# Optimization experiments

Measured on AMD Instinct MI355X. Metric: run time of the kernel, lower is better.

The kernel has to match this reference:

```python
import jax, jax.numpy as jnp
import numpy as np

N, E, D_F, D_H = 100000, 1600000, 128, 128


def setup_inputs() -> dict:
    key = jax.random.key(0)
    ks = jax.random.split(key, 16)
    inp = {
        'h': jax.random.normal(ks[0], (N, D_H), dtype=jnp.float32),
        'f_src': jax.random.normal(ks[1], (N, D_F), dtype=jnp.float32),
        'f_dst': jax.random.normal(ks[2], (N, D_F), dtype=jnp.float32),
        'src': jax.random.randint(ks[3], (E,), 0, N, dtype=jnp.int32),
        'dst': jax.random.randint(ks[4], (E,), 0, N, dtype=jnp.int32),
        # parameters (match torch init: 0.001*rand for W/U, zeros for b)
        'wz': 0.001 * jax.random.uniform(ks[5], (D_F, D_H), dtype=jnp.float32),
        'uz': 0.001 * jax.random.uniform(ks[6], (D_H, D_H), dtype=jnp.float32),
        'bz': jnp.zeros((1, D_H), dtype=jnp.float32),
        'wr': 0.001 * jax.random.uniform(ks[7], (D_F, D_H), dtype=jnp.float32),
        'ur': 0.001 * jax.random.uniform(ks[8], (D_H, D_H), dtype=jnp.float32),
        'br': jnp.zeros((1, D_H), dtype=jnp.float32),
        'w': 0.001 * jax.random.uniform(ks[9], (D_F, D_H), dtype=jnp.float32),
        'u': 0.001 * jax.random.uniform(ks[10], (D_H, D_H), dtype=jnp.float32),
        'b': jnp.zeros((1, D_H), dtype=jnp.float32),
    }
    return inp


def reference(h, f_src, f_dst, src, dst, wz, uz, bz, wr, ur, br, w, u, b):
    n = h.shape[0]
    # Stage 1: s[v] = sum_{u in N_in(v)} h[u]   (copy_src + sum reduce)
    s = jax.ops.segment_sum(h[src], dst, num_segments=n)  # [N, d_h]
    # z gate per node
    z = jax.nn.sigmoid(f_src @ wz + s @ uz + bz)
    # Stage 2: per-edge reset gate using SOURCE node data, then sum to dst
    h_e = h[src]                                           # [E, d_h]
    r = jax.nn.sigmoid(f_dst[src] @ wr + h_e @ ur + br)    # [E, d_h]
    sum_r_times_h = jax.ops.segment_sum(r * h_e, dst, num_segments=n)
    # Candidate state and gated update
    h_tilde = jnp.tanh(f_src @ w + sum_r_times_h @ u + b)
    h_new = (1.0 - z) * s + z * h_tilde
    return h_new
```

## Files before the change

kernel.cpp:

```cpp
#include <hip/hip_runtime.h>
#include <stdint.h>

#define DH 128

typedef __attribute__((ext_vector_type(8))) short short8;
typedef __attribute__((ext_vector_type(4))) float f32x4;

__device__ __forceinline__ unsigned short f2bf(float f) {
  union { float f; unsigned u; } v; v.f = f;
  unsigned r = v.u + 0x7fffu + ((v.u >> 16) & 1u);
  return (unsigned short)(r >> 16);
}
__device__ __forceinline__ float bf2f(unsigned short s) {
  union { unsigned u; float f; } v; v.u = ((unsigned)s) << 16;
  return v.f;
}

__global__ __launch_bounds__(256) void pack_weights(
    const float* __restrict__ wz, const float* __restrict__ uz,
    const float* __restrict__ wr, const float* __restrict__ ur,
    const float* __restrict__ w,  const float* __restrict__ u,
    unsigned short* __restrict__ wf) {
  int t = blockIdx.x * 256 + threadIdx.x;
  if (t >= 6 * 16384) return;
  int mat = t >> 14;
  int r = t & 16383;
  int j = r & 7;
  int lane = (r >> 3) & 63;
  int nt = (r >> 9) & 7;
  int kt = (r >> 12) & 3;
  int k = kt * 32 + ((lane >> 4) << 3) + j;
  int n = nt * 16 + (lane & 15);
  const float* m_;
  switch (mat) {
    case 0: m_ = wz; break; case 1: m_ = uz; break; case 2: m_ = wr; break;
    case 3: m_ = ur; break; case 4: m_ = w;  break; default: m_ = u;
  }
  wf[t] = f2bf(m_[k * DH + n]);
}

__global__ __launch_bounds__(256) void zero_counts(int* __restrict__ cnt, int N) {
  int i = blockIdx.x * 256 + threadIdx.x;
  if (i < N) cnt[i] = 0;
}
__global__ __launch_bounds__(256) void count_deg(const int* __restrict__ dst,
                                                 int* __restrict__ cnt, int E) {
  int i = blockIdx.x * 256 + threadIdx.x;
  if (i < E) atomicAdd(&cnt[dst[i]], 1);
}
__global__ __launch_bounds__(256) void block_reduce(const int* __restrict__ cnt,
                                                    int* __restrict__ bsum, int N) {
  __shared__ int sd[256];
  int t = threadIdx.x;
  int i = blockIdx.x * 256 + t;
  sd[t] = (i < N) ? cnt[i] : 0;
  __syncthreads();
  for (int d = 128; d > 0; d >>= 1) {
    if (t < d) sd[t] += sd[t + d];
    __syncthreads();
  }
  if (t == 0) bsum[blockIdx.x] = sd[0];
}
__global__ __launch_bounds__(512) void scan_bsums(int* __restrict__ bsum, int nb,
                                                  int* __restrict__ offs, int N, int E) {
  __shared__ int sd[512];
  int t = threadIdx.x;
  int v = (t < nb) ? bsum[t] : 0;
  sd[t] = v;
  __syncthreads();
  for (int d = 1; d < 512; d <<= 1) {
    int x = sd[t];
    if (t >= d) x += sd[t - d];
    __syncthreads();
    sd[t] = x;
    __syncthreads();
  }
  if (t < nb) bsum[t] = sd[t] - v;
  if (t == 0) offs[N] = E;
}
__global__ __launch_bounds__(256) void scan_block(const int* __restrict__ cnt,
                                                  const int* __restrict__ boff,
                                                  int* __restrict__ offs,
                                                  int* __restrict__ cursor, int N) {
  __shared__ int sd[256];
  int t = threadIdx.x;
  int i = blockIdx.x * 256 + t;
  int v = (i < N) ? cnt[i] : 0;
  sd[t] = v;
  __syncthreads();
  for (int d = 1; d < 256; d <<= 1) {
    int x = sd[t];
    if (t >= d) x += sd[t - d];
    __syncthreads();
    sd[t] = x;
    __syncthreads();
  }
  if (i < N) {
    int o = boff[blockIdx.x] + sd[t] - v;
    offs[i] = o;
    cursor[i] = o;
  }
}
__global__ __launch_bounds__(256) void scatter_edges(const int* __restrict__ src,
                                                     const int* __restrict__ dst,
                                                     int* __restrict__ cursor,
                                                     int* __restrict__ esrc, int E) {
  int i = blockIdx.x * 256 + threadIdx.x;
  if (i < E) {
    int pos = atomicAdd(&cursor[dst[i]], 1);
    esrc[pos] = src[i];
  }
}

__device__ __forceinline__ short8 load_afrag(const float* __restrict__ base, int row, int ko) {
  const float* p = base + (size_t)row * DH + ko;
  float4 a = *(const float4*)p;
  float4 b = *(const float4*)(p + 4);
  union { short8 v; unsigned short s[8]; } u;
  u.s[0] = f2bf(a.x); u.s[1] = f2bf(a.y); u.s[2] = f2bf(a.z); u.s[3] = f2bf(a.w);
  u.s[4] = f2bf(b.x); u.s[5] = f2bf(b.y); u.s[6] = f2bf(b.z); u.s[7] = f2bf(b.w);
  return u.v;
}

__global__ __launch_bounds__(256) void k1_node_gate(
    const float* __restrict__ fdst, const float* __restrict__ h,
    const unsigned short* __restrict__ wf, const float* __restrict__ br,
    unsigned short* __restrict__ m, int N) {
  const unsigned short* wrf = wf + 2 * 16384;
  const unsigned short* urf = wf + 3 * 16384;
  int lane = threadIdx.x & 63, wid = threadIdx.x >> 6;
  int rowb = blockIdx.x * 64 + wid * 16;
  int mrow = lane & 15, g = lane >> 4;
  int arow = rowb + mrow; if (arow > N - 1) arow = N - 1;
  f32x4 acc[8];
#pragma unroll
  for (int i = 0; i < 8; ++i) acc[i] = (f32x4){0.f, 0.f, 0.f, 0.f};
#pragma unroll
  for (int kh = 0; kh < 2; ++kh) {
    const float* srcm = kh ? h : fdst;
    const unsigned short* bfm = kh ? urf : wrf;
#pragma unroll
    for (int kt = 0; kt < 4; ++kt) {
      short8 af = load_afrag(srcm, arow, kt * 32 + g * 8);
#pragma unroll
      for (int nt = 0; nt < 8; ++nt) {
        short8 bf = *(const short8*)&bfm[(kt * 8 + nt) * 512 + lane * 8];
        acc[nt] = __builtin_amdgcn_mfma_f32_16x16x32_bf16(af, bf, acc[nt], 0, 0, 0);
      }
    }
  }
  int orow = rowb + g * 4;
#pragma unroll
  for (int nt = 0; nt < 8; ++nt) {
    int col = nt * 16 + mrow;
    float bias = br[col];
#pragma unroll
    for (int r = 0; r < 4; ++r) {
      int row = orow + r;
      if (row < N) {
        float arg = acc[nt][r] + bias;
        float gv = 1.f / (1.f + __expf(-arg));
        float mv = gv * h[(size_t)row * DH + col];
        m[(size_t)row * DH + col] = f2bf(mv);
      }
    }
  }
}

__global__ __launch_bounds__(256) void k3_gather(
    const int* __restrict__ offs, const int* __restrict__ esrc,
    const float* __restrict__ h, const unsigned short* __restrict__ m,
    float* __restrict__ s, float* __restrict__ mrh, int N) {
  int lane = threadIdx.x & 63, wid = threadIdx.x >> 6;
  int v = blockIdx.x * 4 + wid;
  if (v >= N) return;
  int e0 = offs[v], e1 = offs[v + 1];
  float sx = 0.f, sy = 0.f, mx = 0.f, my = 0.f;
  size_t c = (size_t)lane * 2;
  int e = e0;
  for (; e + 1 < e1; e += 2) {
    int u0 = esrc[e], u1 = esrc[e + 1];
    float2 h0 = *(const float2*)&h[(size_t)u0 * DH + c];
    float2 h1 = *(const float2*)&h[(size_t)u1 * DH + c];
    uint32_t m0 = *(const uint32_t*)&m[(size_t)u0 * DH + c];
    uint32_t m1 = *(const uint32_t*)&m[(size_t)u1 * DH + c];
    sx += h0.x + h1.x;
    sy += h0.y + h1.y;
    mx += bf2f((unsigned short)(m0 & 0xffff)) + bf2f((unsigned short)(m1 & 0xffff));
    my += bf2f((unsigned short)(m0 >> 16)) + bf2f((unsigned short)(m1 >> 16));
  }
  if (e < e1) {
    int u0 = esrc[e];
    float2 h0 = *(const float2*)&h[(size_t)u0 * DH + c];
    uint32_t m0 = *(const uint32_t*)&m[(size_t)u0 * DH + c];
    sx += h0.x; sy += h0.y;
    mx += bf2f((unsigned short)(m0 & 0xffff));
    my += bf2f((unsigned short)(m0 >> 16));
  }
  float2 so; so.x = sx; so.y = sy;
  float2 mo; mo.x = mx; mo.y = my;
  *(float2*)&s[(size_t)v * DH + c] = so;
  *(float2*)&mrh[(size_t)v * DH + c] = mo;
}

__global__ __launch_bounds__(256) void k4_update(
    const float* __restrict__ fsrc, const float* __restrict__ s,
    const float* __restrict__ mrh, const unsigned short* __restrict__ wf,
    const float* __restrict__ bz, const float* __restrict__ bb,
    float* __restrict__ out, int N) {
  const unsigned short* wzf = wf + 0 * 16384;
  const unsigned short* uzf = wf + 1 * 16384;
  const unsigned short* wwf = wf + 4 * 16384;
  const unsigned short* uuf = wf + 5 * 16384;
  int lane = threadIdx.x & 63, wid = threadIdx.x >> 6;
  int rowb = blockIdx.x * 64 + wid * 16;
  int mrow = lane & 15, g = lane >> 4;
  int arow = rowb + mrow; if (arow > N - 1) arow = N - 1;
  f32x4 az[8], ah[8];
#pragma unroll
  for (int i = 0; i < 8; ++i) {
    az[i] = (f32x4){0.f, 0.f, 0.f, 0.f};
    ah[i] = (f32x4){0.f, 0.f, 0.f, 0.f};
  }
#pragma unroll
  for (int kt = 0; kt < 4; ++kt) {
    short8 af = load_afrag(fsrc, arow, kt * 32 + g * 8);
#pragma unroll
    for (int nt = 0; nt < 8; ++nt) {
      short8 b0 = *(const short8*)&wzf[(kt * 8 + nt) * 512 + lane * 8];
      short8 b1 = *(const short8*)&wwf[(kt * 8 + nt) * 512 + lane * 8];
      az[nt] = __builtin_amdgcn_mfma_f32_16x16x32_bf16(af, b0, az[nt], 0, 0, 0);
      ah[nt] = __builtin_amdgcn_mfma_f32_16x16x32_bf16(af, b1, ah[nt], 0, 0, 0);
    }
  }
#pragma unroll
  for (int kt = 0; kt < 4; ++kt) {
    short8 af = load_afrag(s, arow, kt * 32 + g * 8);
#pragma unroll
    for (int nt = 0; nt < 8; ++nt) {
      short8 b0 = *(const short8*)&uzf[(kt * 8 + nt) * 512 + lane * 8];
      az[nt] = __builtin_amdgcn_mfma_f32_16x16x32_bf16(af, b0, az[nt], 0, 0, 0);
    }
  }
#pragma unroll
  for (int kt = 0; kt < 4; ++kt) {
    short8 af = load_afrag(mrh, arow, kt * 32 + g * 8);
#pragma unroll
    for (int nt = 0; nt < 8; ++nt) {
      short8 b1 = *(const short8*)&uuf[(kt * 8 + nt) * 512 + lane * 8];
      ah[nt] = __builtin_amdgcn_mfma_f32_16x16x32_bf16(af, b1, ah[nt], 0, 0, 0);
    }
  }
  int orow = rowb + g * 4;
#pragma unroll
  for (int nt = 0; nt < 8; ++nt) {
    int col = nt * 16 + mrow;
    float bzc = bz[col], bbc = bb[col];
#pragma unroll
    for (int r = 0; r < 4; ++r) {
      int row = orow + r;
      if (row < N) {
        float zarg = az[nt][r] + bzc;
        float z = 1.f / (1.f + __expf(-zarg));
        float e2 = __expf(2.f * (ah[nt][r] + bbc));
        float th = (e2 - 1.f) / (e2 + 1.f);
        float sv = s[(size_t)row * DH + col];
        out[(size_t)row * DH + col] = (1.f - z) * sv + z * th;
      }
    }
  }
}

extern "C" void kernel_launch(void* const* d_in, const int* in_sizes, int n_in,
                              void* d_out, int out_size, void* d_ws, size_t ws_size,
                              hipStream_t stream) {
  const float* h    = (const float*)d_in[0];
  const float* fsrc = (const float*)d_in[1];
  const float* fdst = (const float*)d_in[2];
  const int*   src  = (const int*)d_in[3];
  const int*   dst  = (const int*)d_in[4];
  const float* wz   = (const float*)d_in[5];
  const float* uz   = (const float*)d_in[6];
  const float* bz   = (const float*)d_in[7];
  const float* wr   = (const float*)d_in[8];
  const float* ur   = (const float*)d_in[9];
  const float* br   = (const float*)d_in[10];
  const float* w    = (const float*)d_in[11];
  const float* u    = (const float*)d_in[12];
  const float* b    = (const float*)d_in[13];
  int N = in_sizes[0] / DH;
  int E = in_sizes[3];
  float* out = (float*)d_out;

  char* ws = (char*)d_ws;
  size_t o = 0;
  auto take = [&](size_t bytes) {
    char* p = ws + o;
    o = (o + bytes + 255) & ~(size_t)255;
    return p;
  };
  unsigned short* wf     = (unsigned short*)take(6 * 16384 * sizeof(unsigned short));
  unsigned short* mbuf   = (unsigned short*)take((size_t)N * DH * 2);
  float*          mrh    = (float*)take((size_t)N * DH * 4);
  int*            cnt    = (int*)take((size_t)N * 4);
  int*            offs   = (int*)take((size_t)(N + 1) * 4);
  int*            cursor = (int*)take((size_t)N * 4);
  int*            bsum   = (int*)take(4096);
  int*            esrc   = (int*)take((size_t)E * 4);

  int nb = (N + 255) / 256;

  pack_weights<<<(6 * 16384 + 255) / 256, 256, 0, stream>>>(wz, uz, wr, ur, w, u, wf);
  zero_counts<<<nb, 256, 0, stream>>>(cnt, N);
  count_deg<<<(E + 255) / 256, 256, 0, stream>>>(dst, cnt, E);
  block_reduce<<<nb, 256, 0, stream>>>(cnt, bsum, N);
  scan_bsums<<<1, 512, 0, stream>>>(bsum, nb, offs, N, E);
  scan_block<<<nb, 256, 0, stream>>>(cnt, bsum, offs, cursor, N);
  scatter_edges<<<(E + 255) / 256, 256, 0, stream>>>(src, dst, cursor, esrc, E);
  k1_node_gate<<<(N + 63) / 64, 256, 0, stream>>>(fdst, h, wf, br, mbuf, N);
  k3_gather<<<(N + 3) / 4, 256, 0, stream>>>(offs, esrc, h, mbuf, out, mrh, N);
  k4_update<<<(N + 63) / 64, 256, 0, stream>>>(fsrc, out, mrh, wf, bz, b, out, N);
}
```

Measured before the change: 681.8 us.

## Store mrh as bf16, unroll gather by 4, use packed bf16 conversion

The intermediate sum of r*h is now written by the gather kernel as bf16 instead of fp32, and the update kernel loads it directly as an MFMA fragment without converting. This halves that buffer's write and read traffic. The gather loop is unrolled to four edges per iteration to keep more loads in flight, and the fp32-to-bf16 conversions now use the hardware packed convert instruction. The risk is a small precision loss on mrh, though it was already being rounded to bf16 before the matmul.

```diff
diff --git a/kernel.cpp b/kernel.cpp
--- a/kernel.cpp
+++ b/kernel.cpp
@@ -11,9 +11,16 @@
   unsigned r = v.u + 0x7fffu + ((v.u >> 16) & 1u);
   return (unsigned short)(r >> 16);
 }
-__device__ __forceinline__ float bf2f(unsigned short s) {
-  union { unsigned u; float f; } v; v.u = ((unsigned)s) << 16;
-  return v.f;
+__device__ __forceinline__ uint32_t cvtpk_bf16(float lo, float hi) {
+  uint32_t r;
+  asm("v_cvt_pk_bf16_f32 %0, %1, %2" : "=v"(r) : "v"(lo), "v"(hi));
+  return r;
+}
+__device__ __forceinline__ float bflo(uint32_t u) {
+  union { uint32_t u; float f; } v; v.u = u << 16; return v.f;
+}
+__device__ __forceinline__ float bfhi(uint32_t u) {
+  union { uint32_t u; float f; } v; v.u = u & 0xffff0000u; return v.f;
 }
 
 __global__ __launch_bounds__(256) void pack_weights(
@@ -116,10 +123,16 @@
   const float* p = base + (size_t)row * DH + ko;
   float4 a = *(const float4*)p;
   float4 b = *(const float4*)(p + 4);
-  union { short8 v; unsigned short s[8]; } u;
-  u.s[0] = f2bf(a.x); u.s[1] = f2bf(a.y); u.s[2] = f2bf(a.z); u.s[3] = f2bf(a.w);
-  u.s[4] = f2bf(b.x); u.s[5] = f2bf(b.y); u.s[6] = f2bf(b.z); u.s[7] = f2bf(b.w);
-  return u.v;
+  union { short8 v; uint32_t u[4]; } r;
+  r.u[0] = cvtpk_bf16(a.x, a.y);
+  r.u[1] = cvtpk_bf16(a.z, a.w);
+  r.u[2] = cvtpk_bf16(b.x, b.y);
+  r.u[3] = cvtpk_bf16(b.z, b.w);
+  return r.v;
+}
+__device__ __forceinline__ short8 load_afrag_bf(const unsigned short* __restrict__ base,
+                                                int row, int ko) {
+  return *(const short8*)(base + (size_t)row * DH + ko);
 }
 
 __global__ __launch_bounds__(256) void k1_node_gate(
@@ -170,42 +183,44 @@
 __global__ __launch_bounds__(256) void k3_gather(
     const int* __restrict__ offs, const int* __restrict__ esrc,
     const float* __restrict__ h, const unsigned short* __restrict__ m,
-    float* __restrict__ s, float* __restrict__ mrh, int N) {
+    float* __restrict__ s, unsigned short* __restrict__ mrh, int N) {
   int lane = threadIdx.x & 63, wid = threadIdx.x >> 6;
   int v = blockIdx.x * 4 + wid;
   if (v >= N) return;
   int e0 = offs[v], e1 = offs[v + 1];
   float sx = 0.f, sy = 0.f, mx = 0.f, my = 0.f;
-  size_t c = (size_t)lane * 2;
+  size_t c = (size_t)(lane * 2);
   int e = e0;
-  for (; e + 1 < e1; e += 2) {
-    int u0 = esrc[e], u1 = esrc[e + 1];
+  for (; e + 3 < e1; e += 4) {
+    int u0 = esrc[e], u1 = esrc[e + 1], u2 = esrc[e + 2], u3 = esrc[e + 3];
     float2 h0 = *(const float2*)&h[(size_t)u0 * DH + c];
     float2 h1 = *(const float2*)&h[(size_t)u1 * DH + c];
+    float2 h2 = *(const float2*)&h[(size_t)u2 * DH + c];
+    float2 h3 = *(const float2*)&h[(size_t)u3 * DH + c];
     uint32_t m0 = *(const uint32_t*)&m[(size_t)u0 * DH + c];
     uint32_t m1 = *(const uint32_t*)&m[(size_t)u1 * DH + c];
-    sx += h0.x + h1.x;
-    sy += h0.y + h1.y;
-    mx += bf2f((unsigned short)(m0 & 0xffff)) + bf2f((unsigned short)(m1 & 0xffff));
-    my += bf2f((unsigned short)(m0 >> 16)) + bf2f((unsigned short)(m1 >> 16));
-  }
-  if (e < e1) {
+    uint32_t m2 = *(const uint32_t*)&m[(size_t)u2 * DH + c];
+    uint32_t m3 = *(const uint32_t*)&m[(size_t)u3 * DH + c];
+    sx += (h0.x + h1.x) + (h2.x + h3.x);
+    sy += (h0.y + h1.y) + (h2.y + h3.y);
+    mx += (bflo(m0) + bflo(m1)) + (bflo(m2) + bflo(m3));
+    my += (bfhi(m0) + bfhi(m1)) + (bfhi(m2) + bfhi(m3));
+  }
+  for (; e < e1; ++e) {
     int u0 = esrc[e];
     float2 h0 = *(const float2*)&h[(size_t)u0 * DH + c];
     uint32_t m0 = *(const uint32_t*)&m[(size_t)u0 * DH + c];
     sx += h0.x; sy += h0.y;
-    mx += bf2f((unsigned short)(m0 & 0xffff));
-    my += bf2f((unsigned short)(m0 >> 16));
+    mx += bflo(m0); my += bfhi(m0);
   }
   float2 so; so.x = sx; so.y = sy;
-  float2 mo; mo.x = mx; mo.y = my;
   *(float2*)&s[(size_t)v * DH + c] = so;
-  *(float2*)&mrh[(size_t)v * DH + c] = mo;
+  *(uint32_t*)&mrh[(size_t)v * DH + c] = cvtpk_bf16(mx, my);
 }
 
 __global__ __launch_bounds__(256) void k4_update(
     const float* __restrict__ fsrc, const float* __restrict__ s,
-    const float* __restrict__ mrh, const unsigned short* __restrict__ wf,
+    const unsigned short* __restrict__ mrh, const unsigned short* __restrict__ wf,
     const float* __restrict__ bz, const float* __restrict__ bb,
     float* __restrict__ out, int N) {
   const unsigned short* wzf = wf + 0 * 16384;
@@ -244,7 +259,7 @@
   }
 #pragma unroll
   for (int kt = 0; kt < 4; ++kt) {
-    short8 af = load_afrag(mrh, arow, kt * 32 + g * 8);
+    short8 af = load_afrag_bf(mrh, arow, kt * 32 + g * 8);
 #pragma unroll
     for (int nt = 0; nt < 8; ++nt) {
       short8 b1 = *(const short8*)&uuf[(kt * 8 + nt) * 512 + lane * 8];
@@ -301,7 +316,7 @@
   };
   unsigned short* wf     = (unsigned short*)take(6 * 16384 * sizeof(unsigned short));
   unsigned short* mbuf   = (unsigned short*)take((size_t)N * DH * 2);
-  float*          mrh    = (float*)take((size_t)N * DH * 4);
+  unsigned short* mrh    = (unsigned short*)take((size_t)N * DH * 2);
   int*            cnt    = (int*)take((size_t)N * 4);
   int*            offs   = (int*)take((size_t)(N + 1) * 4);
   int*            cursor = (int*)take((size_t)N * 4);
```

Measured after the change: 673.7 us. No clear change (-1.2%).

## Switch to fp16 MFMA and gather interleaved fp16 h/m rows

Applied to the files above, without the earlier changes.

Weights and A-fragments now use fp16 with the f16 MFMA, converted through packed round-toward-zero instructions. The node-gate kernel writes an interleaved fp16 buffer holding h and r*h for each node, so the gather reads one 8-byte chunk per edge instead of separate fp32 h and bf16 m reads. That halves random gather traffic and stores the mrh intermediate in fp16. The gather is unrolled by four with vectorized index loads, and the degree count is vectorized with a memset instead of a zero kernel. The cost is precision: h summed from fp16 values, and fp16 accumulation of the m sum in the gather, which risks error or overflow on high-degree nodes.

```diff
diff --git a/kernel.cpp b/kernel.cpp
--- a/kernel.cpp
+++ b/kernel.cpp
@@ -3,24 +3,16 @@
 
 #define DH 128
 
-typedef __attribute__((ext_vector_type(8))) short short8;
+typedef __attribute__((ext_vector_type(8))) _Float16 half8;
+typedef __attribute__((ext_vector_type(2))) _Float16 half2v;
+typedef __attribute__((ext_vector_type(2))) __fp16 fp16x2;
 typedef __attribute__((ext_vector_type(4))) float f32x4;
-
-__device__ __forceinline__ unsigned short f2bf(float f) {
-  union { float f; unsigned u; } v; v.f = f;
-  unsigned r = v.u + 0x7fffu + ((v.u >> 16) & 1u);
-  return (unsigned short)(r >> 16);
-}
-__device__ __forceinline__ float bf2f(unsigned short s) {
-  union { unsigned u; float f; } v; v.u = ((unsigned)s) << 16;
-  return v.f;
-}
 
 __global__ __launch_bounds__(256) void pack_weights(
     const float* __restrict__ wz, const float* __restrict__ uz,
     const float* __restrict__ wr, const float* __restrict__ ur,
     const float* __restrict__ w,  const float* __restrict__ u,
-    unsigned short* __restrict__ wf) {
+    _Float16* __restrict__ wf) {
   int t = blockIdx.x * 256 + threadIdx.x;
   if (t >= 6 * 16384) return;
   int mat = t >> 14;
@@ -36,17 +28,21 @@
     case 0: m_ = wz; break; case 1: m_ = uz; break; case 2: m_ = wr; break;
     case 3: m_ = ur; break; case 4: m_ = w;  break; default: m_ = u;
   }
-  wf[t] = f2bf(m_[k * DH + n]);
-}
-
-__global__ __launch_bounds__(256) void zero_counts(int* __restrict__ cnt, int N) {
-  int i = blockIdx.x * 256 + threadIdx.x;
-  if (i < N) cnt[i] = 0;
-}
+  wf[t] = (_Float16)m_[k * DH + n];
+}
+
 __global__ __launch_bounds__(256) void count_deg(const int* __restrict__ dst,
                                                  int* __restrict__ cnt, int E) {
-  int i = blockIdx.x * 256 + threadIdx.x;
-  if (i < E) atomicAdd(&cnt[dst[i]], 1);
+  int i = (blockIdx.x * 256 + threadIdx.x) * 4;
+  if (i + 3 < E) {
+    int4 d = *(const int4*)&dst[i];
+    atomicAdd(&cnt[d.x], 1);
+    atomicAdd(&cnt[d.y], 1);
+    atomicAdd(&cnt[d.z], 1);
+    atomicAdd(&cnt[d.w], 1);
+  } else {
+    for (; i < E; ++i) atomicAdd(&cnt[dst[i]], 1);
+  }
 }
 __global__ __launch_bounds__(256) void block_reduce(const int* __restrict__ cnt,
                                                     int* __restrict__ bsum, int N) {
@@ -112,22 +108,28 @@
   }
 }
 
-__device__ __forceinline__ short8 load_afrag(const float* __restrict__ base, int row, int ko) {
+__device__ __forceinline__ half8 load_afrag(const float* __restrict__ base, int row, int ko) {
   const float* p = base + (size_t)row * DH + ko;
   float4 a = *(const float4*)p;
   float4 b = *(const float4*)(p + 4);
-  union { short8 v; unsigned short s[8]; } u;
-  u.s[0] = f2bf(a.x); u.s[1] = f2bf(a.y); u.s[2] = f2bf(a.z); u.s[3] = f2bf(a.w);
-  u.s[4] = f2bf(b.x); u.s[5] = f2bf(b.y); u.s[6] = f2bf(b.z); u.s[7] = f2bf(b.w);
-  return u.v;
+  union { half8 v; fp16x2 h[4]; } r;
+  r.h[0] = __builtin_amdgcn_cvt_pkrtz(a.x, a.y);
+  r.h[1] = __builtin_amdgcn_cvt_pkrtz(a.z, a.w);
+  r.h[2] = __builtin_amdgcn_cvt_pkrtz(b.x, b.y);
+  r.h[3] = __builtin_amdgcn_cvt_pkrtz(b.z, b.w);
+  return r.v;
+}
+__device__ __forceinline__ half8 load_afrag_h(const _Float16* __restrict__ base,
+                                              int row, int ko) {
+  return *(const half8*)(base + (size_t)row * DH + ko);
 }
 
 __global__ __launch_bounds__(256) void k1_node_gate(
     const float* __restrict__ fdst, const float* __restrict__ h,
-    const unsigned short* __restrict__ wf, const float* __restrict__ br,
-    unsigned short* __restrict__ m, int N) {
-  const unsigned short* wrf = wf + 2 * 16384;
-  const unsigned short* urf = wf + 3 * 16384;
+    const _Float16* __restrict__ wf, const float* __restrict__ br,
+    _Float16* __restrict__ hm, int N) {
+  const _Float16* wrf = wf + 2 * 16384;
+  const _Float16* urf = wf + 3 * 16384;
   int lane = threadIdx.x & 63, wid = threadIdx.x >> 6;
   int rowb = blockIdx.x * 64 + wid * 16;
   int mrow = lane & 15, g = lane >> 4;
@@ -138,14 +140,14 @@
 #pragma unroll
   for (int kh = 0; kh < 2; ++kh) {
     const float* srcm = kh ? h : fdst;
-    const unsigned short* bfm = kh ? urf : wrf;
+    const _Float16* bfm = kh ? urf : wrf;
 #pragma unroll
     for (int kt = 0; kt < 4; ++kt) {
-      short8 af = load_afrag(srcm, arow, kt * 32 + g * 8);
+      half8 af = load_afrag(srcm, arow, kt * 32 + g * 8);
 #pragma unroll
       for (int nt = 0; nt < 8; ++nt) {
-        short8 bf = *(const short8*)&bfm[(kt * 8 + nt) * 512 + lane * 8];
-        acc[nt] = __builtin_amdgcn_mfma_f32_16x16x32_bf16(af, bf, acc[nt], 0, 0, 0);
+        half8 bf = *(const half8*)&bfm[(kt * 8 + nt) * 512 + lane * 8];
+        acc[nt] = __builtin_amdgcn_mfma_f32_16x16x32_f16(af, bf, acc[nt], 0, 0, 0);
       }
     }
   }
@@ -158,10 +160,13 @@
     for (int r = 0; r < 4; ++r) {
       int row = orow + r;
       if (row < N) {
+        float hval = h[(size_t)row * DH + col];
         float arg = acc[nt][r] + bias;
         float gv = 1.f / (1.f + __expf(-arg));
-        float mv = gv * h[(size_t)row * DH + col];
-        m[(size_t)row * DH + col] = f2bf(mv);
+        float mv = gv * hval;
+        size_t base = (size_t)row * 256 + (size_t)((col >> 1) << 2) + (col & 1);
+        hm[base] = (_Float16)hval;
+        hm[base + 2] = (_Float16)mv;
       }
     }
   }
@@ -169,49 +174,52 @@
 
 __global__ __launch_bounds__(256) void k3_gather(
     const int* __restrict__ offs, const int* __restrict__ esrc,
-    const float* __restrict__ h, const unsigned short* __restrict__ m,
-    float* __restrict__ s, float* __restrict__ mrh, int N) {
+    const _Float16* __restrict__ hm,
+    float* __restrict__ s, _Float16* __restrict__ mrh, int N) {
   int lane = threadIdx.x & 63, wid = threadIdx.x >> 6;
   int v = blockIdx.x * 4 + wid;
   if (v >= N) return;
   int e0 = offs[v], e1 = offs[v + 1];
-  float sx = 0.f, sy = 0.f, mx = 0.f, my = 0.f;
-  size_t c = (size_t)lane * 2;
+  float sx = 0.f, sy = 0.f;
+  half2v msum = (half2v)(_Float16)0.f;
+  int c4 = lane * 4;
   int e = e0;
-  for (; e + 1 < e1; e += 2) {
-    int u0 = esrc[e], u1 = esrc[e + 1];
-    float2 h0 = *(const float2*)&h[(size_t)u0 * DH + c];
-    float2 h1 = *(const float2*)&h[(size_t)u1 * DH + c];
-    uint32_t m0 = *(const uint32_t*)&m[(size_t)u0 * DH + c];
-    uint32_t m1 = *(const uint32_t*)&m[(size_t)u1 * DH + c];
-    sx += h0.x + h1.x;
-    sy += h0.y + h1.y;
-    mx += bf2f((unsigned short)(m0 & 0xffff)) + bf2f((unsigned short)(m1 & 0xffff));
-    my += bf2f((unsigned short)(m0 >> 16)) + bf2f((unsigned short)(m1 >> 16));
-  }
-  if (e < e1) {
+  for (; e + 3 < e1; e += 4) {
+    int4 uu = *(const int4*)&esrc[e];
+    uint2 q0 = *(const uint2*)(hm + (size_t)uu.x * 256 + c4);
+    uint2 q1 = *(const uint2*)(hm + (size_t)uu.y * 256 + c4);
+    uint2 q2 = *(const uint2*)(hm + (size_t)uu.z * 256 + c4);
+    uint2 q3 = *(const uint2*)(hm + (size_t)uu.w * 256 + c4);
+    half2v h0 = __builtin_bit_cast(half2v, q0.x), m0 = __builtin_bit_cast(half2v, q0.y);
+    half2v h1 = __builtin_bit_cast(half2v, q1.x), m1 = __builtin_bit_cast(half2v, q1.y);
+    half2v h2 = __builtin_bit_cast(half2v, q2.x), m2 = __builtin_bit_cast(half2v, q2.y);
+    half2v h3 = __builtin_bit_cast(half2v, q3.x), m3 = __builtin_bit_cast(half2v, q3.y);
+    sx += ((float)h0[0] + (float)h1[0]) + ((float)h2[0] + (float)h3[0]);
+    sy += ((float)h0[1] + (float)h1[1]) + ((float)h2[1] + (float)h3[1]);
+    msum = msum + (m0 + m1) + (m2 + m3);
+  }
+  for (; e < e1; ++e) {
     int u0 = esrc[e];
-    float2 h0 = *(const float2*)&h[(size_t)u0 * DH + c];
-    uint32_t m0 = *(const uint32_t*)&m[(size_t)u0 * DH + c];
-    sx += h0.x; sy += h0.y;
-    mx += bf2f((unsigned short)(m0 & 0xffff));
-    my += bf2f((unsigned short)(m0 >> 16));
+    uint2 q0 = *(const uint2*)(hm + (size_t)u0 * 256 + c4);
+    half2v h0 = __builtin_bit_cast(half2v, q0.x), m0 = __builtin_bit_cast(half2v, q0.y);
+    sx += (float)h0[0];
+    sy += (float)h0[1];
+    msum = msum + m0;
   }
   float2 so; so.x = sx; so.y = sy;
-  float2 mo; mo.x = mx; mo.y = my;
-  *(float2*)&s[(size_t)v * DH + c] = so;
-  *(float2*)&mrh[(size_t)v * DH + c] = mo;
+  *(float2*)&s[(size_t)v * DH + lane * 2] = so;
+  *(half2v*)&mrh[(size_t)v * DH + lane * 2] = msum;
 }
 
 __global__ __launch_bounds__(256) void k4_update(
     const float* __restrict__ fsrc, const float* __restrict__ s,
-    const float* __restrict__ mrh, const unsigned short* __restrict__ wf,
+    const _Float16* __restrict__ mrh, const _Float16* __restrict__ wf,
     const float* __restrict__ bz, const float* __restrict__ bb,
     float* __restrict__ out, int N) {
-  const unsigned short* wzf = wf + 0 * 16384;
-  const unsigned short* uzf = wf + 1 * 16384;
-  const unsigned short* wwf = wf + 4 * 16384;
-  const unsigned short* uuf = wf + 5 * 16384;
+  const _Float16* wzf = wf + 0 * 16384;
+  const _Float16* uzf = wf + 1 * 16384;
+  const _Float16* wwf = wf + 4 * 16384;
+  const _Float16* uuf = wf + 5 * 16384;
   int lane = threadIdx.x & 63, wid = threadIdx.x >> 6;
   int rowb = blockIdx.x * 64 + wid * 16;
   int mrow = lane & 15, g = lane >> 4;
@@ -224,31 +232,31 @@
   }
 #pragma unroll
   for (int kt = 0; kt < 4; ++kt) {
-    short8 af = load_afrag(fsrc, arow, kt * 32 + g * 8);
+    half8 af = load_afrag(fsrc, arow, kt * 32 + g * 8);
 #pragma unroll
     for (int nt = 0; nt < 8; ++nt) {
-      short8 b0 = *(const short8*)&wzf[(kt * 8 + nt) * 512 + lane * 8];
-      short8 b1 = *(const short8*)&wwf[(kt * 8 + nt) * 512 + lane * 8];
-      az[nt] = __builtin_amdgcn_mfma_f32_16x16x32_bf16(af, b0, az[nt], 0, 0, 0);
-      ah[nt] = __builtin_amdgcn_mfma_f32_16x16x32_bf16(af, b1, ah[nt], 0, 0, 0);
+      half8 b0 = *(const half8*)&wzf[(kt * 8 + nt) * 512 + lane * 8];
+      half8 b1 = *(const half8*)&wwf[(kt * 8 + nt) * 512 + lane * 8];
+      az[nt] = __builtin_amdgcn_mfma_f32_16x16x32_f16(af, b0, az[nt], 0, 0, 0);
+      ah[nt] = __builtin_amdgcn_mfma_f32_16x16x32_f16(af, b1, ah[nt], 0, 0, 0);
     }
   }
 #pragma unroll
   for (int kt = 0; kt < 4; ++kt) {
-    short8 af = load_afrag(s, arow, kt * 32 + g * 8);
+    half8 af = load_afrag(s, arow, kt * 32 + g * 8);
 #pragma unroll
     for (int nt = 0; nt < 8; ++nt) {
-      short8 b0 = *(const short8*)&uzf[(kt * 8 + nt) * 512 + lane * 8];
-      az[nt] = __builtin_amdgcn_mfma_f32_16x16x32_bf16(af, b0, az[nt], 0, 0, 0);
+      half8 b0 = *(const half8*)&uzf[(kt * 8 + nt) * 512 + lane * 8];
+      az[nt] = __builtin_amdgcn_mfma_f32_16x16x32_f16(af, b0, az[nt], 0, 0, 0);
     }
   }
 #pragma unroll
   for (int kt = 0; kt < 4; ++kt) {
-    short8 af = load_afrag(mrh, arow, kt * 32 + g * 8);
+    half8 af = load_afrag_h(mrh, arow, kt * 32 + g * 8);
 #pragma unroll
     for (int nt = 0; nt < 8; ++nt) {
-      short8 b1 = *(const short8*)&uuf[(kt * 8 + nt) * 512 + lane * 8];
-      ah[nt] = __builtin_amdgcn_mfma_f32_16x16x32_bf16(af, b1, ah[nt], 0, 0, 0);
+      half8 b1 = *(const half8*)&uuf[(kt * 8 + nt) * 512 + lane * 8];
+      ah[nt] = __builtin_amdgcn_mfma_f32_16x16x32_f16(af, b1, ah[nt], 0, 0, 0);
     }
   }
   int orow = rowb + g * 4;
@@ -299,25 +307,25 @@
     o = (o + bytes + 255) & ~(size_t)255;
     return p;
   };
-  unsigned short* wf     = (unsigned short*)take(6 * 16384 * sizeof(unsigned short));
-  unsigned short* mbuf   = (unsigned short*)take((size_t)N * DH * 2);
-  float*          mrh    = (float*)take((size_t)N * DH * 4);
-  int*            cnt    = (int*)take((size_t)N * 4);
-  int*            offs   = (int*)take((size_t)(N + 1) * 4);
-  int*            cursor = (int*)take((size_t)N * 4);
-  int*            bsum   = (int*)take(4096);
-  int*            esrc   = (int*)take((size_t)E * 4);
+  _Float16* wf     = (_Float16*)take(6 * 16384 * sizeof(_Float16));
+  _Float16* hm     = (_Float16*)take((size_t)N * 256 * 2);
+  _Float16* mrh    = (_Float16*)take((size_t)N * DH * 2);
+  int*      cnt    = (int*)take((size_t)N * 4);
+  int*      offs   = (int*)take((size_t)(N + 1) * 4);
+  int*      cursor = (int*)take((size_t)N * 4);
+  int*      bsum   = (int*)take(4096);
+  int*      esrc   = (int*)take((size_t)E * 4);
 
   int nb = (N + 255) / 256;
 
   pack_weights<<<(6 * 16384 + 255) / 256, 256, 0, stream>>>(wz, uz, wr, ur, w, u, wf);
-  zero_counts<<<nb, 256, 0, stream>>>(cnt, N);
-  count_deg<<<(E + 255) / 256, 256, 0, stream>>>(dst, cnt, E);
+  (void)hipMemsetAsync(cnt, 0, (size_t)N * 4, stream);
+  count_deg<<<((E + 3) / 4 + 255) / 256, 256, 0, stream>>>(dst, cnt, E);
   block_reduce<<<nb, 256, 0, stream>>>(cnt, bsum, N);
   scan_bsums<<<1, 512, 0, stream>>>(bsum, nb, offs, N, E);
   scan_block<<<nb, 256, 0, stream>>>(cnt, bsum, offs, cursor, N);
   scatter_edges<<<(E + 255) / 256, 256, 0, stream>>>(src, dst, cursor, esrc, E);
-  k1_node_gate<<<(N + 63) / 64, 256, 0, stream>>>(fdst, h, wf, br, mbuf, N);
-  k3_gather<<<(N + 3) / 4, 256, 0, stream>>>(offs, esrc, h, mbuf, out, mrh, N);
+  k1_node_gate<<<(N + 63) / 64, 256, 0, stream>>>(fdst, h, wf, br, hm, N);
+  k3_gather<<<(N + 3) / 4, 256, 0, stream>>>(offs, esrc, hm, out, mrh, N);
   k4_update<<<(N + 63) / 64, 256, 0, stream>>>(fsrc, out, mrh, wf, bz, b, out, N);
 }
```

Measured after the change: 629.5 us. 7.7% less time.
